# Performance work log

Hardware: AMD Instinct MI355X
Metric: run time of the kernel (lower is better)

The kernel has to match this reference:

```python
import jax, jax.numpy as jnp
import numpy as np

B, S, N_CATE, N_CONT = 32, 1024, 4, 4
HIDDEN, ATTN, VOCAB, EMB = 1024, 512, 1000, 128


def sinusoidal_pe(seq_len, d_model, base=10000.0):
    pos = jnp.arange(seq_len, dtype=jnp.float32)[:, None]            # [S,1]
    i = jnp.arange(d_model // 2, dtype=jnp.float32)[None, :]         # [1,D/2]
    ang = pos / jnp.power(base, 2.0 * i / d_model)                   # [S,D/2]
    pe = jnp.zeros((seq_len, d_model), dtype=jnp.float32)
    pe = pe.at[:, 0::2].set(jnp.sin(ang))
    pe = pe.at[:, 1::2].set(jnp.cos(ang))
    return pe


def setup_inputs() -> dict:
    key = jax.random.key(0)
    ks = jax.random.split(key, 20)
    s = 0.02
    inp = {
        "cate_x": jax.random.randint(ks[0], (B, S, N_CATE), 0, VOCAB, dtype=jnp.int64)
                  if jax.config.read("jax_enable_x64") else
                  jax.random.randint(ks[0], (B, S, N_CATE), 0, VOCAB, dtype=jnp.int32),
        "cont_x": jax.random.normal(ks[1], (B, S, N_CONT), dtype=jnp.float32),
        "mask": jnp.ones((B, S), dtype=bool),
        "targets": jax.random.uniform(ks[2], (B, S), dtype=jnp.float32),
        # EntireEmbedding params: 4 cate tables + cont linear + comb projection
        "E0": jax.random.normal(ks[3], (VOCAB, EMB), dtype=jnp.float32) * s,
        "E1": jax.random.normal(ks[4], (VOCAB, EMB), dtype=jnp.float32) * s,
        "E2": jax.random.normal(ks[5], (VOCAB, EMB), dtype=jnp.float32) * s,
        "E3": jax.random.normal(ks[6], (VOCAB, EMB), dtype=jnp.float32) * s,
        "Wc": jax.random.normal(ks[7], (N_CONT, N_CATE * EMB), dtype=jnp.float32) * s,
        "Wproj": jax.random.normal(ks[8], (2 * N_CATE * EMB, HIDDEN), dtype=jnp.float32) * s,
        # two-head attention linears (bias=False)
        "WQ1": jax.random.normal(ks[9], (HIDDEN, ATTN), dtype=jnp.float32) * s,
        "WK1": jax.random.normal(ks[10], (HIDDEN, ATTN), dtype=jnp.float32) * s,
        "WV1": jax.random.normal(ks[11], (HIDDEN, ATTN), dtype=jnp.float32) * s,
        "WQ2": jax.random.normal(ks[12], (HIDDEN, ATTN), dtype=jnp.float32) * s,
        "WK2": jax.random.normal(ks[13], (HIDDEN, ATTN), dtype=jnp.float32) * s,
        "WV2": jax.random.normal(ks[14], (HIDDEN, ATTN), dtype=jnp.float32) * s,
        "W0": jax.random.normal(ks[15], (2 * ATTN, HIDDEN), dtype=jnp.float32) * s,
        "Wf": jax.random.normal(ks[16], (HIDDEN, 1), dtype=jnp.float32) * s,
    }
    return inp


def _attend(x, WQ, WK, WV):
    Q = x @ WQ  # [B,S,A]
    K = x @ WK
    V = x @ WV
    scores = jnp.einsum("bqd,bkd->bqk", Q, K) / jnp.sqrt(jnp.float32(ATTN))
    # faithful to nn.Softmax(dim=1): normalize over the QUERY axis
    attn = jax.nn.softmax(scores, axis=1)
    return jnp.einsum("bqk,bkv->bqv", attn, V)


def reference(cate_x, cont_x, mask, targets, E0, E1, E2, E3, Wc, Wproj,
              WQ1, WK1, WV1, WQ2, WK2, WV2, W0, Wf):
    # EntireEmbedding: per-feature cate embeddings + cont projection -> comb proj
    cate_emb = jnp.concatenate(
        [E0[cate_x[..., 0]], E1[cate_x[..., 1]], E2[cate_x[..., 2]], E3[cate_x[..., 3]]],
        axis=-1)                                   # [B,S,512]
    cont_emb = cont_x @ Wc                          # [B,S,512]
    x = jnp.concatenate([cate_emb, cont_emb], axis=-1) @ Wproj  # [B,S,H]
    x = x + sinusoidal_pe(x.shape[1], HIDDEN)[None, :, :]
    z1 = _attend(x, WQ1, WK1, WV1)                  # [B,S,A]
    z2 = _attend(x, WQ2, WK2, WV2)                  # [B,S,A]
    z = jnp.concatenate([z1, z2], axis=-1) @ W0     # [B,S,H]
    out = jax.nn.sigmoid(z @ Wf)                    # FinalConnecting: Linear(H,1)+sigmoid
    return out.squeeze(-1)                          # [B,S]
```

## Files before the change

### kernel.cpp

```cpp
#include <hip/hip_runtime.h>
#include <hip/hip_bf16.h>
#include <math.h>

#define BB    32
#define SS    1024
#define HID   1024
#define AT    512
#define NVOC  1000
#define NT    (BB*SS)

typedef unsigned short u16;
typedef __attribute__((ext_vector_type(8))) short s16x8;
typedef __attribute__((ext_vector_type(4))) float f32x4;

__device__ __forceinline__ float bf2f(u16 u) {
    union { unsigned int i; float f; } x; x.i = ((unsigned int)u) << 16; return x.f;
}
__device__ __forceinline__ u16 f2bf(float f) {
    union { float f; unsigned int i; } u; u.f = f;
    unsigned int r = u.i + 0x7fffu + ((u.i >> 16) & 1u);
    return (u16)(r >> 16);
}
__device__ __forceinline__ float4 ld4(const float* p) { return *(const float4*)p; }
__device__ __forceinline__ float4 ld4bf(const u16* p) {
    ushort4 v = *(const ushort4*)p;
    return make_float4(bf2f(v.x), bf2f(v.y), bf2f(v.z), bf2f(v.w));
}
__device__ __forceinline__ void unpack8(uint4 v, float* x) {
    x[0] = bf2f((u16)(v.x & 0xffff)); x[1] = bf2f((u16)(v.x >> 16));
    x[2] = bf2f((u16)(v.y & 0xffff)); x[3] = bf2f((u16)(v.y >> 16));
    x[4] = bf2f((u16)(v.z & 0xffff)); x[5] = bf2f((u16)(v.z >> 16));
    x[6] = bf2f((u16)(v.w & 0xffff)); x[7] = bf2f((u16)(v.w >> 16));
}

__device__ __forceinline__ void gld16(const u16* g, u16* l) {
    __builtin_amdgcn_global_load_lds(
        (const __attribute__((address_space(1))) unsigned int*)g,
        (__attribute__((address_space(3))) unsigned int*)l,
        16, 0, 0);
}

struct Ptrs4f { const float* p[4]; };

__device__ __forceinline__ float blockReduceSum(float x) {
    #pragma unroll
    for (int off = 32; off > 0; off >>= 1) x += __shfl_down(x, off, 64);
    __shared__ float tmp[4];
    int lane = threadIdx.x & 63, wid = threadIdx.x >> 6;
    if (lane == 0) tmp[wid] = x;
    __syncthreads();
    if (threadIdx.x == 0) x = tmp[0] + tmp[1] + tmp[2] + tmp[3];
    return x;
}
__device__ __forceinline__ float waveReduceSum(float x) {
    #pragma unroll
    for (int off = 32; off > 0; off >>= 1) x += __shfl_down(x, off, 64);
    return x;
}

__global__ void k_s1(Ptrs4f E, const float* __restrict__ Wproj, Ptrs4f W,
                     const float* __restrict__ W0, const float* __restrict__ Wf,
                     u16* __restrict__ PE16, u16* __restrict__ E16o, u16* __restrict__ Wp16,
                     u16* __restrict__ Wt, float* __restrict__ W0f,
                     float* __restrict__ Wcp, float* __restrict__ CQ) {
    int blk = blockIdx.x, tid = threadIdx.x;
    if (blk < 2048) {
        int idx = blk*256 + tid;
        int s = idx >> 9, i = idx & 511;
        const float l2_10000 = 13.287712379549449f;
        float denom = exp2f((2.f * (float)i / 1024.f) * l2_10000);
        float ang = (float)s / denom;
        unsigned int pack = ((unsigned int)f2bf(cosf(ang)) << 16) | f2bf(sinf(ang));
        *(unsigned int*)(PE16 + (size_t)s*1024 + 2*i) = pack;
    } else if (blk < 4048) {
        int id2 = blk - 2048;
        int f = id2 / 500;
        int i = (id2 % 500)*256 + tid;
        E16o[(size_t)f*128000 + i] = f2bf(E.p[f][i]);
    } else if (blk < 6096) {
        int i = (blk - 4048)*256 + tid;
        Wp16[i] = f2bf(Wproj[i]);
    } else if (blk < 8144) {
        int tb = blk - 6096;
        int mat = tb >> 9, t2 = tb & 511;
        int cx = t2 & 15, ry = t2 >> 4;
        int r0 = ry*32, c0 = cx*32;
        const float* in = W.p[mat];
        u16* out = Wt + (size_t)mat*1024*512;
        __shared__ float tt[32][33];
        int tx = tid & 31, ty8 = tid >> 5;
        #pragma unroll
        for (int it = 0; it < 4; ++it)
            tt[ty8 + it*8][tx] = in[(size_t)(r0 + ty8 + it*8)*512 + c0 + tx];
        __syncthreads();
        #pragma unroll
        for (int it = 0; it < 4; ++it)
            out[(size_t)(c0 + ty8 + it*8)*1024 + r0 + tx] = f2bf(tt[tx][ty8 + it*8]);
    } else if (blk < 9168) {
        int row = blk - 8144;
        const float* rp = W0 + (size_t)row*1024;
        float a = 0.f;
        for (int j = tid; j < 1024; j += 256) a += rp[j] * Wf[j];
        a = blockReduceSum(a);
        if (tid == 0) W0f[row] = a;
    } else {
        int idx = (blk - 9168)*256 + tid;
        if (idx < 4096) Wcp[idx] = 0.f;
        else CQ[idx - 4096] = 0.f;
    }
}

__global__ void k_s2(const float* __restrict__ Wc, const float* __restrict__ Wproj,
                     Ptrs4f W, const float* __restrict__ WV1, const float* __restrict__ WV2,
                     const float* __restrict__ W0f, float* __restrict__ Wcp, float* __restrict__ v) {
    int blk = blockIdx.x, tid = threadIdx.x;
    if (blk < 64) {
        int c = blk >> 4, ic = (blk >> 2) & 3, jc = blk & 3;
        int i = ic*256 + tid;
        float a = 0.f;
        for (int j = jc*128; j < jc*128 + 128; ++j)
            a += Wc[c*512 + j] * Wproj[(size_t)(512 + j)*1024 + i];
        atomicAdd(&Wcp[c*1024 + i], a);
    } else {
        int b2 = blk - 64;
        int h = b2 >> 10, i = b2 & 1023;
        const float* WV = h ? WV2 : WV1;
        const float* wf = W0f + h*512;
        float a = 0.f;
        for (int aa = tid; aa < 512; aa += 256) a += WV[(size_t)i*512 + aa] * wf[aa];
        a = blockReduceSum(a);
        if (tid == 0) v[h*1024 + i] = a;
    }
}

__device__ __forceinline__ void cstore(float* p, float v) { *p = v; }
__device__ __forceinline__ void cstore(u16* p, float v)   { *p = f2bf(v); }

template<typename CT, bool CTRANS>
__device__ __forceinline__ void mfma_gemm(const u16* __restrict__ A, const u16* __restrict__ B,
                                          CT* __restrict__ C, int M, int N, int K, float alpha,
                                          int m0, int n0) {
    __shared__ u16 As[128*64];
    __shared__ u16 Bs[128*64];
    const int tid = threadIdx.x;
    const int wave = tid >> 6, lane = tid & 63;
    const int quad = lane >> 4, l16 = lane & 15;
    const int wm = (wave >> 1)*64, wn = (wave & 1)*64;
    const int srow = lane >> 3;
    const int scol = ((lane & 7) ^ srow) * 8;
    f32x4 acc[4][4] = {};

    for (int k0 = 0; k0 < K; k0 += 64) {
        #pragma unroll
        for (int p = 0; p < 4; ++p) {
            int rb = wave*32 + p*8;
            gld16(A + (size_t)(m0 + rb + srow)*K + k0 + scol, As + rb*64);
            gld16(B + (size_t)(n0 + rb + srow)*K + k0 + scol, Bs + rb*64);
        }
        __syncthreads();
        #pragma unroll
        for (int kk = 0; kk < 2; ++kk) {
            s16x8 af[4], bf[4];
            #pragma unroll
            for (int i = 0; i < 4; ++i) {
                int row = wm + i*16 + l16;
                af[i] = *(const s16x8*)(As + row*64 + (((kk*4 + quad) ^ (row & 7)) * 8));
            }
            #pragma unroll
            for (int j = 0; j < 4; ++j) {
                int row = wn + j*16 + l16;
                bf[j] = *(const s16x8*)(Bs + row*64 + (((kk*4 + quad) ^ (row & 7)) * 8));
            }
            #pragma unroll
            for (int i = 0; i < 4; ++i)
                #pragma unroll
                for (int j = 0; j < 4; ++j)
                    acc[i][j] = __builtin_amdgcn_mfma_f32_16x16x32_bf16(af[i], bf[j], acc[i][j], 0, 0, 0);
        }
        __syncthreads();
    }
    #pragma unroll
    for (int i = 0; i < 4; ++i) {
        #pragma unroll
        for (int r = 0; r < 4; ++r) {
            int gm = m0 + wm + i*16 + quad*4 + r;
            if (gm < M) {
                #pragma unroll
                for (int j = 0; j < 4; ++j) {
                    int gn = n0 + wn + j*16 + l16;
                    if (CTRANS) cstore(C + (size_t)gn*M + gm, acc[i][j][r] * alpha);
                    else        cstore(C + (size_t)gm*N + gn, acc[i][j][r] * alpha);
                }
            }
        }
    }
}

__global__ __launch_bounds__(256) void k_s3(const u16* __restrict__ Wp16, const u16* __restrict__ Wt,
                                            u16* __restrict__ PWT,
                                            Ptrs4f W, const float* __restrict__ Wcp, float* __restrict__ CQ,
                                            const float* __restrict__ Wproj, const float* __restrict__ v,
                                            float* __restrict__ pv) {
    int blk = blockIdx.x, tid = threadIdx.x;
    if (blk < 64) {
        int x = blk & 3, z = blk >> 2;
        int f = z >> 2, w = z & 3;
        mfma_gemm<u16,true>(Wp16 + (size_t)f*128*1024, Wt + (size_t)w*512*1024,
                            PWT + (size_t)z*512*128, 128, 512, 1024, 1.f, 0, x*128);
    } else if (blk < 320) {
        int r = blk - 64;
        int ns = r & 1, wc = (r >> 1) & 15, jc = r >> 5;
        int w = wc & 3, c = wc >> 2; int n = ns*256 + tid;
        const float* Ww = W.p[w];
        float a = 0.f;
        for (int j = jc*128; j < jc*128 + 128; ++j) a += Wcp[c*1024 + j] * Ww[(size_t)j*512 + n];
        atomicAdd(&CQ[(size_t)(w*4 + c)*512 + n], a);
    } else {
        int b2 = blk - 320;
        int i = b2 & 127, fh = b2 >> 7; int f = fh >> 1, h = fh & 1;
        const float* row = Wproj + (size_t)(f*128 + i)*1024;
        const float* vh = v + h*1024;
        float a = 0.f;
        for (int j = tid; j < 1024; j += 256) a += row[j] * vh[j];
        a = blockReduceSum(a);
        if (tid == 0) pv[(size_t)fh*128 + i] = a;
    }
}

__global__ __launch_bounds__(256) void k_s4(const u16* __restrict__ E16, const u16* __restrict__ PWT,
                                            const u16* __restrict__ PE16, const u16* __restrict__ Wt,
                                            u16* __restrict__ TQK16, u16* __restrict__ PEQ16,
                                            const float* __restrict__ Wcp, const float* __restrict__ v,
                                            const float* __restrict__ pv,
                                            float* __restrict__ Ut, float* __restrict__ pu, float* __restrict__ cu) {
    int blk = blockIdx.x;
    if (blk < 640) {
        int z = blk >> 5, r = blk & 31, y = r >> 2, x = r & 3;
        if (z < 16) {
            int f = z >> 2;
            mfma_gemm<u16,false>(E16 + (size_t)f*128000, PWT + (size_t)z*512*128,
                       TQK16 + (size_t)z*1000*512, 1000, 512, 128, 1.f, y*128, x*128);
        } else {
            int w = z - 16;
            mfma_gemm<u16,false>(PE16, Wt + (size_t)w*512*1024, PEQ16 + (size_t)w*1024*512,
                       1024, 512, 1024, 1.f, y*128, x*128);
        }
        return;
    }
    int id = blk - 640;
    if (id < 2000) {
        int wave = threadIdx.x >> 6, lane = threadIdx.x & 63;
        int d = id*4 + wave;
        int f = d / 2000, h = (d / 1000) & 1, r = d % 1000;
        unsigned int e2 = *(const unsigned int*)(E16 + ((size_t)f*1000 + r)*128 + lane*2);
        const float* pvp = pv + (size_t)(f*2 + h)*128 + lane*2;
        float a = bf2f((u16)(e2 & 0xffff)) * pvp[0] + bf2f((u16)(e2 >> 16)) * pvp[1];
        a = waveReduceSum(a);
        if (lane == 0) Ut[(size_t)(f*2 + h)*1000 + r] = a;
    } else if (id < 4048) {
        int tq = id - 2000; int h = tq >> 10, s = tq & 1023;
        float4 a = ld4bf(PE16 + (size_t)s*1024 + threadIdx.x*4);
        float4 b = ld4(v + h*1024 + threadIdx.x*4);
        float p = a.x*b.x + a.y*b.y + a.z*b.z + a.w*b.w;
        p = blockReduceSum(p);
        if (threadIdx.x == 0) pu[h*1024 + s] = p;
    } else {
        int tq = id - 4048; int h = tq >> 2, c = tq & 3;
        float4 a = ld4(Wcp + c*1024 + threadIdx.x*4);
        float4 b = ld4(v + h*1024 + threadIdx.x*4);
        float p = a.x*b.x + a.y*b.y + a.z*b.z + a.w*b.w;
        p = blockReduceSum(p);
        if (threadIdx.x == 0) cu[h*4 + c] = p;
    }
}

__global__ __launch_bounds__(512, 2) void k_g_S256(
        const u16* __restrict__ Q, const u16* __restrict__ K,
        u16* __restrict__ Sb, float alpha,
        float* __restrict__ Pm, float* __restrict__ Pd, int b0) {
    __shared__ u16 As[2][16384];
    __shared__ u16 Bs[2][16384];
    const int tid = threadIdx.x;
    const int wave = tid >> 6, lane = tid & 63;
    const int quad = lane >> 4, l16 = lane & 15;
    const int wm = wave >> 2, wn = wave & 3;

    const int nwg = (int)gridDim.x;
    int fblk = (int)blockIdx.x;
    int qq = nwg >> 3, rr = nwg & 7;
    int xcd = fblk & 7, idx = fblk >> 3;
    int swz = (xcd < rr ? xcd*(qq + 1) : rr*(qq + 1) + (xcd - rr)*qq) + idx;
    int b = swz >> 4, tile = swz & 15;
    int m0 = (tile >> 2) << 8, n0 = (tile & 3) << 8;

    const u16* __restrict__ Ab = Q + (size_t)b*SS*AT;
    const u16* __restrict__ Bb = K + (size_t)b*SS*AT;
    u16* __restrict__ C = Sb + (size_t)b*SS*SS;

    const int srow = lane >> 3;
    const int scol = ((lane & 7) ^ srow) * 8;

    f32x4 acc[8][4] = {};

    auto stage = [&](int kt, int bf) {
        const u16* ap = Ab + (size_t)(m0 + wave*8 + srow)*AT + kt*64 + scol;
        const u16* bp = Bb + (size_t)(n0 + wave*8 + srow)*AT + kt*64 + scol;
        u16* la = &As[bf][wave*8*64];
        u16* lb = &Bs[bf][wave*8*64];
        #pragma unroll
        for (int p = 0; p < 4; ++p) {
            gld16(ap + (size_t)p*64*AT, la + p*64*64);
            gld16(bp + (size_t)p*64*AT, lb + p*64*64);
        }
    };

    auto compute = [&](int bf) {
        s16x8 bfr[4][2];
        #pragma unroll
        for (int j = 0; j < 4; ++j) {
            int row = wn*64 + j*16 + l16;
            #pragma unroll
            for (int kk = 0; kk < 2; ++kk)
                bfr[j][kk] = *(const s16x8*)(&Bs[bf][row*64 + (((kk*4 + quad) ^ (row & 7)) * 8)]);
        }
        #pragma unroll
        for (int ib = 0; ib < 2; ++ib) {
            s16x8 afr[4][2];
            #pragma unroll
            for (int i2 = 0; i2 < 4; ++i2) {
                int row = wm*128 + (ib*4 + i2)*16 + l16;
                #pragma unroll
                for (int kk = 0; kk < 2; ++kk)
                    afr[i2][kk] = *(const s16x8*)(&As[bf][row*64 + (((kk*4 + quad) ^ (row & 7)) * 8)]);
            }
            __builtin_amdgcn_s_setprio(1);
            #pragma unroll
            for (int i2 = 0; i2 < 4; ++i2) {
                #pragma unroll
                for (int j = 0; j < 4; ++j) {
                    acc[ib*4+i2][j] = __builtin_amdgcn_mfma_f32_16x16x32_bf16(afr[i2][0], bfr[j][0], acc[ib*4+i2][j], 0, 0, 0);
                    acc[ib*4+i2][j] = __builtin_amdgcn_mfma_f32_16x16x32_bf16(afr[i2][1], bfr[j][1], acc[ib*4+i2][j], 0, 0, 0);
                }
            }
            __builtin_amdgcn_s_setprio(0);
        }
    };

    stage(0, 0);
    stage(1, 1);
    asm volatile("s_waitcnt vmcnt(8)" ::: "memory");
    __builtin_amdgcn_s_barrier();

    #pragma unroll
    for (int t = 0; t < 8; ++t) {
        compute(t & 1);
        asm volatile("" ::: "memory");
        __builtin_amdgcn_s_barrier();
        if (t < 6) {
            stage(t + 2, t & 1);
            asm volatile("s_waitcnt vmcnt(8)" ::: "memory");
        } else if (t == 6) {
            asm volatile("s_waitcnt vmcnt(0)" ::: "memory");
        }
        __builtin_amdgcn_sched_barrier(0);
        __builtin_amdgcn_s_barrier();
    }

    #pragma unroll
    for (int i = 0; i < 8; ++i) {
        #pragma unroll
        for (int r = 0; r < 4; ++r) {
            int gm = m0 + wm*128 + i*16 + quad*4 + r;
            u16 q0 = f2bf(acc[i][0][r] * alpha);
            u16 q1 = f2bf(acc[i][1][r] * alpha);
            u16 q2 = f2bf(acc[i][2][r] * alpha);
            u16 q3 = f2bf(acc[i][3][r] * alpha);
            acc[i][0][r] = bf2f(q0); acc[i][1][r] = bf2f(q1);
            acc[i][2][r] = bf2f(q2); acc[i][3][r] = bf2f(q3);
            unsigned int lo = (unsigned int)q0 | ((unsigned int)q1 << 16);
            unsigned int hi = (unsigned int)q2 | ((unsigned int)q3 << 16);
            *(uint2*)(C + (size_t)gm*SS + n0 + wn*64 + l16*4) = make_uint2(lo, hi);
        }
    }
    float* sM = (float*)&As[0][0];
    float* sS = (float*)&Bs[0][0];
    #pragma unroll
    for (int j = 0; j < 4; ++j) {
        float mx = -3.4e38f;
        #pragma unroll
        for (int i = 0; i < 8; ++i)
            #pragma unroll
            for (int r = 0; r < 4; ++r) mx = fmaxf(mx, acc[i][j][r]);
        mx = fmaxf(mx, __shfl_xor(mx, 16, 64));
        mx = fmaxf(mx, __shfl_xor(mx, 32, 64));
        float sm = 0.f;
        #pragma unroll
        for (int i = 0; i < 8; ++i)
            #pragma unroll
            for (int r = 0; r < 4; ++r) sm += exp2f(acc[i][j][r] - mx);
        sm += __shfl_xor(sm, 16, 64);
        sm += __shfl_xor(sm, 32, 64);
        if (quad == 0) { sM[wave*64 + j*16 + l16] = mx; sS[wave*64 + j*16 + l16] = sm; }
    }
    __syncthreads();
    if (tid < 256) {
        int c = tid, wq = c >> 6, cc = c & 63;
        float ma = sM[wq*64 + cc],       sa = sS[wq*64 + cc];
        float mb = sM[(4 + wq)*64 + cc], sb2 = sS[(4 + wq)*64 + cc];
        float mm = fmaxf(ma, mb);
        float ss = sa * exp2f(ma - mm) + sb2 * exp2f(mb - mm);
        size_t po = ((size_t)(b0 + b)*4 + (m0 >> 8))*1024;
        Pm[po + n0 + c] = mm;
        Pd[po + n0 + c] = ss;
    }
}

__global__ void k_gather(const int* __restrict__ cate, const float* __restrict__ cont,
                         const u16* __restrict__ TQK, const float* __restrict__ CQ,
                         const u16* __restrict__ PEQ, const float* __restrict__ Ut,
                         const float* __restrict__ cu, const float* __restrict__ pu,
                         u16* __restrict__ Qh, u16* __restrict__ Kh,
                         float* __restrict__ u, int h) {
    int tid = threadIdx.x;
    size_t t = (size_t)blockIdx.x*2 + (tid >> 7);
    int r = tid & 127;
    int s = (int)(t & 1023);
    int4 cc = *(const int4*)(cate + t*4);
    float4 cv = ld4(cont + t*4);
    int e = r >> 6;
    int w = 2*h + e;
    int n = (r & 63)*8;
    const u16* t0 = TQK + ((size_t)(0*4  + w)*1000 + cc.x)*512 + n;
    const u16* t1 = TQK + ((size_t)(1*4  + w)*1000 + cc.y)*512 + n;
    const u16* t2 = TQK + ((size_t)(2*4  + w)*1000 + cc.z)*512 + n;
    const u16* t3 = TQK + ((size_t)(3*4  + w)*1000 + cc.w)*512 + n;
    const u16* pq = PEQ + ((size_t)w*1024 + s)*512 + n;
    const float* cq = CQ + (size_t)w*2048 + n;
    float a0[8], a1[8], a2[8], a3[8], ap[8];
    unpack8(*(const uint4*)t0, a0); unpack8(*(const uint4*)t1, a1);
    unpack8(*(const uint4*)t2, a2); unpack8(*(const uint4*)t3, a3);
    unpack8(*(const uint4*)pq, ap);
    unsigned int pack[4];
    #pragma unroll
    for (int jp = 0; jp < 4; ++jp) {
        float x0, x1;
        #pragma unroll
        for (int half = 0; half < 2; ++half) {
            int j = jp*2 + half;
            float x = a0[j] + a1[j] + a2[j] + a3[j] + ap[j]
                    + cv.x*cq[j] + cv.y*cq[512+j] + cv.z*cq[1024+j] + cv.w*cq[1536+j];
            if (half == 0) x0 = x; else x1 = x;
        }
        pack[jp] = ((unsigned int)f2bf(x1) << 16) | f2bf(x0);
    }
    u16* op = (e ? Kh : Qh) + t*512 + n;
    *(uint4*)op = make_uint4(pack[0], pack[1], pack[2], pack[3]);
    if (r == 0) {
        float uu = pu[h*1024 + s]
                 + Ut[(0*2 + h)*1000 + cc.x] + Ut[(1*2 + h)*1000 + cc.y]
                 + Ut[(2*2 + h)*1000 + cc.z] + Ut[(3*2 + h)*1000 + cc.w]
                 + cv.x*cu[h*4+0] + cv.y*cu[h*4+1] + cv.z*cu[h*4+2] + cv.w*cu[h*4+3];
        u[(size_t)h*NT + t] = uu;
    }
}

__global__ void k_stats_combine(const float* __restrict__ Pm, const float* __restrict__ Pd,
                                const float* __restrict__ u, float* __restrict__ wexp, int b0) {
    int idx = b0*1024 + blockIdx.x*256 + threadIdx.x;
    int b = idx >> 10, k = idx & 1023;
    float mx = -3.4e38f;
    #pragma unroll
    for (int mt = 0; mt < 4; ++mt) mx = fmaxf(mx, Pm[((size_t)b*4 + mt)*1024 + k]);
    float dd = 0.f;
    #pragma unroll
    for (int mt = 0; mt < 4; ++mt) dd += Pd[((size_t)b*4 + mt)*1024 + k]
                                       * exp2f(Pm[((size_t)b*4 + mt)*1024 + k] - mx);
    int q = (k & ~63) | (((k & 15) << 2) | ((k & 63) >> 4));
    wexp[((size_t)b << 10) + q] = u[idx] / dd * exp2f(-mx);
}

__global__ void k_logit(const u16* __restrict__ Sb, const float* __restrict__ wexp,
                        float* __restrict__ logits, float* __restrict__ out,
                        int b0, int mode) {
    int wave = threadIdx.x >> 6, lane = threadIdx.x & 63;
    size_t bi = (size_t)(gridDim.x - 1 - blockIdx.x);
    size_t tl = bi*4 + wave;
    size_t tabs = (size_t)b0*1024 + tl;
    int b = (int)(tabs >> 10);
    const u16* row = Sb + tl*1024;
    const float* wb = wexp + ((size_t)b << 10);
    float acc = 0.f;
    #pragma unroll
    for (int half = 0; half < 2; ++half) {
        int k = lane*8 + half*512;
        float sv[8];
        unpack8(*(const uint4*)(row + k), sv);
        float4 w0 = ld4(wb + k), w1 = ld4(wb + k + 4);
        acc += exp2f(sv[0])*w0.x + exp2f(sv[1])*w0.y + exp2f(sv[2])*w0.z + exp2f(sv[3])*w0.w
             + exp2f(sv[4])*w1.x + exp2f(sv[5])*w1.y + exp2f(sv[6])*w1.z + exp2f(sv[7])*w1.w;
    }
    acc = waveReduceSum(acc);
    if (lane == 0) {
        if (mode == 0) logits[tabs] = acc;
        else {
            float x = logits[tabs] + acc;
            out[tabs] = 1.f / (1.f + expf(-x));
        }
    }
}

extern "C" void kernel_launch(void* const* d_in, const int* in_sizes, int n_in,
                              void* d_out, int out_size, void* d_ws, size_t ws_size,
                              hipStream_t stream) {
    const int*   cate = (const int*)d_in[0];
    const float* cont = (const float*)d_in[1];
    Ptrs4f E; E.p[0] = (const float*)d_in[4]; E.p[1] = (const float*)d_in[5];
              E.p[2] = (const float*)d_in[6]; E.p[3] = (const float*)d_in[7];
    const float* Wc    = (const float*)d_in[8];
    const float* Wproj = (const float*)d_in[9];
    Ptrs4f W; W.p[0] = (const float*)d_in[10];
              W.p[1] = (const float*)d_in[11];
              W.p[2] = (const float*)d_in[13];
              W.p[3] = (const float*)d_in[14];
    const float* WV1 = (const float*)d_in[12];
    const float* WV2 = (const float*)d_in[15];
    const float* W0  = (const float*)d_in[16];
    const float* Wf  = (const float*)d_in[17];

    char* base = (char*)d_ws;
    size_t off = 0;
    auto alloc = [&](size_t bytes) { void* p = base + off; off += (bytes + 255) & ~(size_t)255; return p; };
    u16*   PE16  = (u16*)  alloc(1048576ull*2);
    u16*   E16   = (u16*)  alloc(4ull*1000*128*2);
    u16*   Wt    = (u16*)  alloc(4ull*512*1024*2);
    u16*   Wp16  = (u16*)  alloc(512ull*1024*2);
    u16*   PWT   = (u16*)  alloc(16ull*512*128*2);
    u16*   TQK16 = (u16*)  alloc(16ull*1000*512*2);
    u16*   PEQ16 = (u16*)  alloc(4ull*1024*512*2);
    float* Wcp   = (float*)alloc(4*1024*4);
    float* W0f   = (float*)alloc(1024*4);
    float* vv    = (float*)alloc(2*1024*4);
    float* CQ    = (float*)alloc(16*512*4);
    float* pvb   = (float*)alloc(8*128*4);
    float* Ut    = (float*)alloc(8*1000*4);
    float* cu    = (float*)alloc(8*4);
    float* pu    = (float*)alloc(2*1024*4);
    float* ubuf  = (float*)alloc(2ull*NT*4);
    u16*   Qh    = (u16*)  alloc((size_t)NT*512*2);
    u16*   Kh    = (u16*)  alloc((size_t)NT*512*2);
    float* Pm    = (float*)alloc(32ull*8*1024*4);
    float* Pd    = (float*)alloc(32ull*8*1024*4);
    float* wbuf  = (float*)alloc(32*1024*4);
    float* logits= (float*)alloc((size_t)NT*4);
    size_t sChunkBytes = (size_t)SS*SS*2;
    size_t remain = (ws_size > off) ? (ws_size - off) : 0;
    int NB = (int)(remain / sChunkBytes);
    if (NB > 32) NB = 32;
    if (NB < 1) NB = 1;
    u16* Sbuf = (u16*)(base + off);

    const float alpha = 0.06375954951107036f;

    k_s1<<<9216, 256, 0, stream>>>(E, Wproj, W, W0, Wf, PE16, E16, Wp16, Wt, W0f, Wcp, CQ);
    k_s2<<<2112, 256, 0, stream>>>(Wc, Wproj, W, WV1, WV2, W0f, Wcp, vv);
    k_s3<<<1344, 256, 0, stream>>>(Wp16, Wt, PWT, W, Wcp, CQ, Wproj, vv, pvb);
    k_s4<<<4696, 256, 0, stream>>>(E16, PWT, PE16, Wt, TQK16, PEQ16, Wcp, vv, pvb, Ut, pu, cu);

    for (int h = 0; h < 2; ++h) {
        k_gather<<<NT/2, 256, 0, stream>>>(cate, cont, TQK16, CQ, PEQ16, Ut, cu, pu, Qh, Kh, ubuf, h);
        for (int b0 = 0; b0 < 32; b0 += NB) {
            int nb = (32 - b0 < NB) ? (32 - b0) : NB;
            k_g_S256<<<16*nb, 512, 0, stream>>>(Qh + (size_t)b0*SS*AT, Kh + (size_t)b0*SS*AT,
                                                Sbuf, alpha, Pm, Pd, b0);
            k_stats_combine<<<nb*4, 256, 0, stream>>>(Pm, Pd, ubuf + (size_t)h*NT, wbuf, b0);
            k_logit<<<nb*256, 256, 0, stream>>>(Sbuf, wbuf, logits, (float*)d_out, b0, h);
        }
    }
}
```

Baseline: 365.3 us.

## Split scores GEMM K-loop into four sub-phases interleaving global loads with MFMA

```diff
diff --git a/kernel.cpp b/kernel.cpp
--- a/kernel.cpp
+++ b/kernel.cpp
@@ -302,67 +302,88 @@
 
     f32x4 acc[8][4] = {};
 
-    auto stage = [&](int kt, int bf) {
-        const u16* ap = Ab + (size_t)(m0 + wave*8 + srow)*AT + kt*64 + scol;
-        const u16* bp = Bb + (size_t)(n0 + wave*8 + srow)*AT + kt*64 + scol;
-        u16* la = &As[bf][wave*8*64];
-        u16* lb = &Bs[bf][wave*8*64];
-        #pragma unroll
-        for (int p = 0; p < 4; ++p) {
-            gld16(ap + (size_t)p*64*AT, la + p*64*64);
-            gld16(bp + (size_t)p*64*AT, lb + p*64*64);
-        }
+    auto stageA = [&](int kt, int q) {
+        gld16(Ab + (size_t)(m0 + q*64 + wave*8 + srow)*AT + kt*64 + scol,
+              &As[kt & 1][q*4096 + wave*512]);
     };
-
-    auto compute = [&](int bf) {
-        s16x8 bfr[4][2];
-        #pragma unroll
-        for (int j = 0; j < 4; ++j) {
+    auto stageB = [&](int kt, int q) {
+        gld16(Bb + (size_t)(n0 + q*64 + wave*8 + srow)*AT + kt*64 + scol,
+              &Bs[kt & 1][q*4096 + wave*512]);
+    };
+
+    s16x8 af[4][2];
+    s16x8 bf[4][2];
+
+    auto readA = [&](int c, int ih) {
+        #pragma unroll
+        for (int i2 = 0; i2 < 4; ++i2) {
+            int row = wm*128 + (ih*4 + i2)*16 + l16;
+            #pragma unroll
+            for (int kk = 0; kk < 2; ++kk)
+                af[i2][kk] = *(const s16x8*)(&As[c][row*64 + (((kk*4 + quad) ^ (row & 7)) * 8)]);
+        }
+    };
+    auto readB2 = [&](int c, int jh) {
+        #pragma unroll
+        for (int j2 = 0; j2 < 2; ++j2) {
+            int j = jh*2 + j2;
             int row = wn*64 + j*16 + l16;
             #pragma unroll
             for (int kk = 0; kk < 2; ++kk)
-                bfr[j][kk] = *(const s16x8*)(&Bs[bf][row*64 + (((kk*4 + quad) ^ (row & 7)) * 8)]);
-        }
-        #pragma unroll
-        for (int ib = 0; ib < 2; ++ib) {
-            s16x8 afr[4][2];
-            #pragma unroll
-            for (int i2 = 0; i2 < 4; ++i2) {
-                int row = wm*128 + (ib*4 + i2)*16 + l16;
-                #pragma unroll
-                for (int kk = 0; kk < 2; ++kk)
-                    afr[i2][kk] = *(const s16x8*)(&As[bf][row*64 + (((kk*4 + quad) ^ (row & 7)) * 8)]);
+                bf[j][kk] = *(const s16x8*)(&Bs[c][row*64 + (((kk*4 + quad) ^ (row & 7)) * 8)]);
+        }
+    };
+    auto mma16 = [&](int ih, int jh) {
+        __builtin_amdgcn_s_setprio(1);
+        #pragma unroll
+        for (int i2 = 0; i2 < 4; ++i2)
+            #pragma unroll
+            for (int j2 = 0; j2 < 2; ++j2) {
+                int i = ih*4 + i2, j = jh*2 + j2;
+                acc[i][j] = __builtin_amdgcn_mfma_f32_16x16x32_bf16(af[i2][0], bf[j][0], acc[i][j], 0, 0, 0);
+                acc[i][j] = __builtin_amdgcn_mfma_f32_16x16x32_bf16(af[i2][1], bf[j][1], acc[i][j], 0, 0, 0);
             }
-            __builtin_amdgcn_s_setprio(1);
-            #pragma unroll
-            for (int i2 = 0; i2 < 4; ++i2) {
-                #pragma unroll
-                for (int j = 0; j < 4; ++j) {
-                    acc[ib*4+i2][j] = __builtin_amdgcn_mfma_f32_16x16x32_bf16(afr[i2][0], bfr[j][0], acc[ib*4+i2][j], 0, 0, 0);
-                    acc[ib*4+i2][j] = __builtin_amdgcn_mfma_f32_16x16x32_bf16(afr[i2][1], bfr[j][1], acc[ib*4+i2][j], 0, 0, 0);
-                }
-            }
-            __builtin_amdgcn_s_setprio(0);
-        }
+        __builtin_amdgcn_s_setprio(0);
     };
-
-    stage(0, 0);
-    stage(1, 1);
-    asm volatile("s_waitcnt vmcnt(8)" ::: "memory");
+    auto midsync = [&]() {
+        __builtin_amdgcn_s_barrier();
+        asm volatile("s_waitcnt lgkmcnt(0)" ::: "memory");
+        __builtin_amdgcn_sched_barrier(0);
+    };
+
+    #pragma unroll
+    for (int q = 0; q < 4; ++q) stageA(0, q);
+    #pragma unroll
+    for (int q = 0; q < 4; ++q) stageB(0, q);
+    stageA(1, 0); stageA(1, 2);
+    stageB(1, 0); stageB(1, 1); stageB(1, 2); stageB(1, 3);
+    asm volatile("s_waitcnt vmcnt(6)" ::: "memory");
     __builtin_amdgcn_s_barrier();
 
     #pragma unroll
     for (int t = 0; t < 8; ++t) {
-        compute(t & 1);
-        asm volatile("" ::: "memory");
+        const int c = t & 1;
+        readA(c, 0);
+        readB2(c, 0);
+        if (t <= 6) { stageA(t + 1, 1); stageA(t + 1, 3); }
+        midsync();
+        mma16(0, 0);
         __builtin_amdgcn_s_barrier();
-        if (t < 6) {
-            stage(t + 2, t & 1);
-            asm volatile("s_waitcnt vmcnt(8)" ::: "memory");
-        } else if (t == 6) {
-            asm volatile("s_waitcnt vmcnt(0)" ::: "memory");
-        }
-        __builtin_amdgcn_sched_barrier(0);
+        readB2(c, 1);
+        if (t <= 5) { stageA(t + 2, 0); stageA(t + 2, 2); }
+        midsync();
+        mma16(0, 1);
+        __builtin_amdgcn_s_barrier();
+        readA(c, 1);
+        if (t <= 5) { stageB(t + 2, 0); stageB(t + 2, 1); }
+        midsync();
+        mma16(1, 0);
+        __builtin_amdgcn_s_barrier();
+        if (t <= 5) { stageB(t + 2, 2); stageB(t + 2, 3); }
+        midsync();
+        mma16(1, 1);
+        if (t <= 5)      asm volatile("s_waitcnt vmcnt(6)" ::: "memory");
+        else if (t == 6) asm volatile("s_waitcnt vmcnt(0)" ::: "memory");
         __builtin_amdgcn_s_barrier();
     }
 
```

Result: faster. 357.8 us (-2.0%).

## Restructure QK^T GEMM into 128-row stripes with triple-buffered streaming K chunks

Applied to the files above, without the earlier changes.

```diff
diff --git a/kernel.cpp b/kernel.cpp
--- a/kernel.cpp
+++ b/kernel.cpp
@@ -70,7 +70,7 @@
         const float l2_10000 = 13.287712379549449f;
         float denom = exp2f((2.f * (float)i / 1024.f) * l2_10000);
         float ang = (float)s / denom;
-        unsigned int pack = ((unsigned int)f2bf(cosf(ang)) << 16) | f2bf(sinf(ang));
+        unsigned int pack = ((unsigned int)f2bf(__cosf(ang)) << 16) | f2bf(__sinf(ang));
         *(unsigned int*)(PE16 + (size_t)s*1024 + 2*i) = pack;
     } else if (blk < 4048) {
         int id2 = blk - 2048;
@@ -278,8 +278,10 @@
         const u16* __restrict__ Q, const u16* __restrict__ K,
         u16* __restrict__ Sb, float alpha,
         float* __restrict__ Pm, float* __restrict__ Pd, int b0) {
-    __shared__ u16 As[2][16384];
-    __shared__ u16 Bs[2][16384];
+    __shared__ u16 As[3][128*64];
+    __shared__ u16 Bs[3][256*64];
+    __shared__ float sM[8][64];
+    __shared__ float sS[8][64];
     const int tid = threadIdx.x;
     const int wave = tid >> 6, lane = tid & 63;
     const int quad = lane >> 4, l16 = lane & 15;
@@ -290,128 +292,143 @@
     int qq = nwg >> 3, rr = nwg & 7;
     int xcd = fblk & 7, idx = fblk >> 3;
     int swz = (xcd < rr ? xcd*(qq + 1) : rr*(qq + 1) + (xcd - rr)*qq) + idx;
-    int b = swz >> 4, tile = swz & 15;
-    int m0 = (tile >> 2) << 8, n0 = (tile & 3) << 8;
-
-    const u16* __restrict__ Ab = Q + (size_t)b*SS*AT;
+    int b = swz >> 3, ms = swz & 7;
+
+    const u16* __restrict__ Ab = Q + (size_t)b*SS*AT + (size_t)ms*128*AT;
     const u16* __restrict__ Bb = K + (size_t)b*SS*AT;
     u16* __restrict__ C = Sb + (size_t)b*SS*SS;
 
     const int srow = lane >> 3;
     const int scol = ((lane & 7) ^ srow) * 8;
 
-    f32x4 acc[8][4] = {};
-
-    auto stage = [&](int kt, int bf) {
-        const u16* ap = Ab + (size_t)(m0 + wave*8 + srow)*AT + kt*64 + scol;
-        const u16* bp = Bb + (size_t)(n0 + wave*8 + srow)*AT + kt*64 + scol;
-        u16* la = &As[bf][wave*8*64];
-        u16* lb = &Bs[bf][wave*8*64];
-        #pragma unroll
-        for (int p = 0; p < 4; ++p) {
-            gld16(ap + (size_t)p*64*AT, la + p*64*64);
-            gld16(bp + (size_t)p*64*AT, lb + p*64*64);
-        }
+    f32x4 acc[4][4] = {};
+
+    auto stage = [&](int t) {
+        int buf = t % 3;
+        int ch = t >> 3, kt = t & 7;
+        const u16* ap = Ab + (size_t)(wave*8 + srow)*AT + kt*64 + scol;
+        const u16* bp = Bb + (size_t)(ch*256 + wave*8 + srow)*AT + kt*64 + scol;
+        #pragma unroll
+        for (int p = 0; p < 2; ++p)
+            gld16(ap + (size_t)p*64*AT, &As[buf][p*4096 + wave*512]);
+        #pragma unroll
+        for (int p = 0; p < 4; ++p)
+            gld16(bp + (size_t)p*64*AT, &Bs[buf][p*4096 + wave*512]);
     };
 
-    auto compute = [&](int bf) {
-        s16x8 bfr[4][2];
-        #pragma unroll
-        for (int j = 0; j < 4; ++j) {
+    stage(0); stage(1);
+    asm volatile("s_waitcnt vmcnt(6)" ::: "memory");
+    __builtin_amdgcn_s_barrier();
+
+    for (int t = 0; t < 32; ++t) {
+        const int buf = t % 3;
+        const u16* Ac = &As[buf][0];
+        const u16* Bc = &Bs[buf][0];
+        s16x8 af[4][2], bf[4][2];
+        #pragma unroll
+        for (int i2 = 0; i2 < 4; ++i2) {
+            int row = wm*64 + i2*16 + l16;
+            #pragma unroll
+            for (int kk = 0; kk < 2; ++kk)
+                af[i2][kk] = *(const s16x8*)(Ac + row*64 + (((kk*4 + quad) ^ (row & 7)) * 8));
+        }
+        #pragma unroll
+        for (int j = 0; j < 2; ++j) {
             int row = wn*64 + j*16 + l16;
             #pragma unroll
             for (int kk = 0; kk < 2; ++kk)
-                bfr[j][kk] = *(const s16x8*)(&Bs[bf][row*64 + (((kk*4 + quad) ^ (row & 7)) * 8)]);
-        }
-        #pragma unroll
-        for (int ib = 0; ib < 2; ++ib) {
-            s16x8 afr[4][2];
-            #pragma unroll
-            for (int i2 = 0; i2 < 4; ++i2) {
-                int row = wm*128 + (ib*4 + i2)*16 + l16;
+                bf[j][kk] = *(const s16x8*)(Bc + row*64 + (((kk*4 + quad) ^ (row & 7)) * 8));
+        }
+        if (t < 30) stage(t + 2);
+        __builtin_amdgcn_s_barrier();
+        asm volatile("s_waitcnt lgkmcnt(0)" ::: "memory");
+        __builtin_amdgcn_sched_barrier(0);
+        __builtin_amdgcn_s_setprio(1);
+        #pragma unroll
+        for (int i2 = 0; i2 < 4; ++i2)
+            #pragma unroll
+            for (int j = 0; j < 2; ++j) {
+                acc[i2][j] = __builtin_amdgcn_mfma_f32_16x16x32_bf16(af[i2][0], bf[j][0], acc[i2][j], 0, 0, 0);
+                acc[i2][j] = __builtin_amdgcn_mfma_f32_16x16x32_bf16(af[i2][1], bf[j][1], acc[i2][j], 0, 0, 0);
+            }
+        __builtin_amdgcn_s_setprio(0);
+        __builtin_amdgcn_s_barrier();
+        #pragma unroll
+        for (int j = 2; j < 4; ++j) {
+            int row = wn*64 + j*16 + l16;
+            #pragma unroll
+            for (int kk = 0; kk < 2; ++kk)
+                bf[j][kk] = *(const s16x8*)(Bc + row*64 + (((kk*4 + quad) ^ (row & 7)) * 8));
+        }
+        __builtin_amdgcn_s_barrier();
+        asm volatile("s_waitcnt lgkmcnt(0)" ::: "memory");
+        __builtin_amdgcn_sched_barrier(0);
+        __builtin_amdgcn_s_setprio(1);
+        #pragma unroll
+        for (int i2 = 0; i2 < 4; ++i2)
+            #pragma unroll
+            for (int j = 2; j < 4; ++j) {
+                acc[i2][j] = __builtin_amdgcn_mfma_f32_16x16x32_bf16(af[i2][0], bf[j][0], acc[i2][j], 0, 0, 0);
+                acc[i2][j] = __builtin_amdgcn_mfma_f32_16x16x32_bf16(af[i2][1], bf[j][1], acc[i2][j], 0, 0, 0);
+            }
+        __builtin_amdgcn_s_setprio(0);
+        if (t < 30)       asm volatile("s_waitcnt vmcnt(6)" ::: "memory");
+        else if (t == 30) asm volatile("s_waitcnt vmcnt(0)" ::: "memory");
+        __builtin_amdgcn_s_barrier();
+
+        if ((t & 7) == 7) {
+            int ch = t >> 3;
+            #pragma unroll
+            for (int i = 0; i < 4; ++i) {
                 #pragma unroll
-                for (int kk = 0; kk < 2; ++kk)
-                    afr[i2][kk] = *(const s16x8*)(&As[bf][row*64 + (((kk*4 + quad) ^ (row & 7)) * 8)]);
-            }
-            __builtin_amdgcn_s_setprio(1);
-            #pragma unroll
-            for (int i2 = 0; i2 < 4; ++i2) {
+                for (int r = 0; r < 4; ++r) {
+                    int gm = ms*128 + wm*64 + i*16 + quad*4 + r;
+                    u16 q0 = f2bf(acc[i][0][r] * alpha);
+                    u16 q1 = f2bf(acc[i][1][r] * alpha);
+                    u16 q2 = f2bf(acc[i][2][r] * alpha);
+                    u16 q3 = f2bf(acc[i][3][r] * alpha);
+                    acc[i][0][r] = bf2f(q0); acc[i][1][r] = bf2f(q1);
+                    acc[i][2][r] = bf2f(q2); acc[i][3][r] = bf2f(q3);
+                    unsigned int lo = (unsigned int)q0 | ((unsigned int)q1 << 16);
+                    unsigned int hi = (unsigned int)q2 | ((unsigned int)q3 << 16);
+                    *(uint2*)(C + (size_t)gm*SS + ch*256 + wn*64 + l16*4) = make_uint2(lo, hi);
+                }
+            }
+            #pragma unroll
+            for (int j = 0; j < 4; ++j) {
+                float mx = -3.4e38f;
                 #pragma unroll
-                for (int j = 0; j < 4; ++j) {
-                    acc[ib*4+i2][j] = __builtin_amdgcn_mfma_f32_16x16x32_bf16(afr[i2][0], bfr[j][0], acc[ib*4+i2][j], 0, 0, 0);
-                    acc[ib*4+i2][j] = __builtin_amdgcn_mfma_f32_16x16x32_bf16(afr[i2][1], bfr[j][1], acc[ib*4+i2][j], 0, 0, 0);
-                }
-            }
-            __builtin_amdgcn_s_setprio(0);
-        }
-    };
-
-    stage(0, 0);
-    stage(1, 1);
-    asm volatile("s_waitcnt vmcnt(8)" ::: "memory");
-    __builtin_amdgcn_s_barrier();
-
-    #pragma unroll
-    for (int t = 0; t < 8; ++t) {
-        compute(t & 1);
-        asm volatile("" ::: "memory");
-        __builtin_amdgcn_s_barrier();
-        if (t < 6) {
-            stage(t + 2, t & 1);
-            asm volatile("s_waitcnt vmcnt(8)" ::: "memory");
-        } else if (t == 6) {
-            asm volatile("s_waitcnt vmcnt(0)" ::: "memory");
-        }
-        __builtin_amdgcn_sched_barrier(0);
-        __builtin_amdgcn_s_barrier();
-    }
-
-    #pragma unroll
-    for (int i = 0; i < 8; ++i) {
-        #pragma unroll
-        for (int r = 0; r < 4; ++r) {
-            int gm = m0 + wm*128 + i*16 + quad*4 + r;
-            u16 q0 = f2bf(acc[i][0][r] * alpha);
-            u16 q1 = f2bf(acc[i][1][r] * alpha);
-            u16 q2 = f2bf(acc[i][2][r] * alpha);
-            u16 q3 = f2bf(acc[i][3][r] * alpha);
-            acc[i][0][r] = bf2f(q0); acc[i][1][r] = bf2f(q1);
-            acc[i][2][r] = bf2f(q2); acc[i][3][r] = bf2f(q3);
-            unsigned int lo = (unsigned int)q0 | ((unsigned int)q1 << 16);
-            unsigned int hi = (unsigned int)q2 | ((unsigned int)q3 << 16);
-            *(uint2*)(C + (size_t)gm*SS + n0 + wn*64 + l16*4) = make_uint2(lo, hi);
-        }
-    }
-    float* sM = (float*)&As[0][0];
-    float* sS = (float*)&Bs[0][0];
-    #pragma unroll
-    for (int j = 0; j < 4; ++j) {
-        float mx = -3.4e38f;
-        #pragma unroll
-        for (int i = 0; i < 8; ++i)
-            #pragma unroll
-            for (int r = 0; r < 4; ++r) mx = fmaxf(mx, acc[i][j][r]);
-        mx = fmaxf(mx, __shfl_xor(mx, 16, 64));
-        mx = fmaxf(mx, __shfl_xor(mx, 32, 64));
-        float sm = 0.f;
-        #pragma unroll
-        for (int i = 0; i < 8; ++i)
-            #pragma unroll
-            for (int r = 0; r < 4; ++r) sm += exp2f(acc[i][j][r] - mx);
-        sm += __shfl_xor(sm, 16, 64);
-        sm += __shfl_xor(sm, 32, 64);
-        if (quad == 0) { sM[wave*64 + j*16 + l16] = mx; sS[wave*64 + j*16 + l16] = sm; }
-    }
-    __syncthreads();
-    if (tid < 256) {
-        int c = tid, wq = c >> 6, cc = c & 63;
-        float ma = sM[wq*64 + cc],       sa = sS[wq*64 + cc];
-        float mb = sM[(4 + wq)*64 + cc], sb2 = sS[(4 + wq)*64 + cc];
-        float mm = fmaxf(ma, mb);
-        float ss = sa * exp2f(ma - mm) + sb2 * exp2f(mb - mm);
-        size_t po = ((size_t)(b0 + b)*4 + (m0 >> 8))*1024;
-        Pm[po + n0 + c] = mm;
-        Pd[po + n0 + c] = ss;
+                for (int i = 0; i < 4; ++i)
+                    #pragma unroll
+                    for (int r = 0; r < 4; ++r) mx = fmaxf(mx, acc[i][j][r]);
+                mx = fmaxf(mx, __shfl_xor(mx, 16, 64));
+                mx = fmaxf(mx, __shfl_xor(mx, 32, 64));
+                float sm = 0.f;
+                #pragma unroll
+                for (int i = 0; i < 4; ++i)
+                    #pragma unroll
+                    for (int r = 0; r < 4; ++r) sm += exp2f(acc[i][j][r] - mx);
+                sm += __shfl_xor(sm, 16, 64);
+                sm += __shfl_xor(sm, 32, 64);
+                if (quad == 0) { sM[wave][j*16 + l16] = mx; sS[wave][j*16 + l16] = sm; }
+            }
+            #pragma unroll
+            for (int i = 0; i < 4; ++i)
+                #pragma unroll
+                for (int j = 0; j < 4; ++j) acc[i][j] = {};
+            __syncthreads();
+            if (tid < 256) {
+                int wn2 = tid >> 6, cc = tid & 63;
+                float ma = sM[wn2][cc],     sa = sS[wn2][cc];
+                float mb = sM[wn2 + 4][cc], sb2 = sS[wn2 + 4][cc];
+                float mm = fmaxf(ma, mb);
+                float ss = sa * exp2f(ma - mm) + sb2 * exp2f(mb - mm);
+                size_t po = ((size_t)(b0 + b)*8 + ms)*1024 + ch*256;
+                Pm[po + tid] = mm;
+                Pd[po + tid] = ss;
+            }
+            __syncthreads();
+        }
     }
 }
 
@@ -470,11 +487,11 @@
     int b = idx >> 10, k = idx & 1023;
     float mx = -3.4e38f;
     #pragma unroll
-    for (int mt = 0; mt < 4; ++mt) mx = fmaxf(mx, Pm[((size_t)b*4 + mt)*1024 + k]);
+    for (int mt = 0; mt < 8; ++mt) mx = fmaxf(mx, Pm[((size_t)b*8 + mt)*1024 + k]);
     float dd = 0.f;
     #pragma unroll
-    for (int mt = 0; mt < 4; ++mt) dd += Pd[((size_t)b*4 + mt)*1024 + k]
-                                       * exp2f(Pm[((size_t)b*4 + mt)*1024 + k] - mx);
+    for (int mt = 0; mt < 8; ++mt) dd += Pd[((size_t)b*8 + mt)*1024 + k]
+                                       * exp2f(Pm[((size_t)b*8 + mt)*1024 + k] - mx);
     int q = (k & ~63) | (((k & 15) << 2) | ((k & 63) >> 4));
     wexp[((size_t)b << 10) + q] = u[idx] / dd * exp2f(-mx);
 }
@@ -570,8 +587,8 @@
         k_gather<<<NT/2, 256, 0, stream>>>(cate, cont, TQK16, CQ, PEQ16, Ut, cu, pu, Qh, Kh, ubuf, h);
         for (int b0 = 0; b0 < 32; b0 += NB) {
             int nb = (32 - b0 < NB) ? (32 - b0) : NB;
-            k_g_S256<<<16*nb, 512, 0, stream>>>(Qh + (size_t)b0*SS*AT, Kh + (size_t)b0*SS*AT,
-                                                Sbuf, alpha, Pm, Pd, b0);
+            k_g_S256<<<8*nb, 512, 0, stream>>>(Qh + (size_t)b0*SS*AT, Kh + (size_t)b0*SS*AT,
+                                               Sbuf, alpha, Pm, Pd, b0);
             k_stats_combine<<<nb*4, 256, 0, stream>>>(Pm, Pd, ubuf + (size_t)h*NT, wbuf, b0);
             k_logit<<<nb*256, 256, 0, stream>>>(Sbuf, wbuf, logits, (float*)d_out, b0, h);
         }
```

Result: slower. 400.3 us (+9.6%).
